# Kernel optimization log

Measured on AMD Instinct MI355X. Metric: run time of the kernel, lower is better.

## Reference

```python
import jax, jax.numpy as jnp
import numpy as np

B, N, D, H, FF, K, L = 8, 4096, 128, 8, 512, 16, 2
DH = D // H
EPS = 1e-5


def setup_inputs() -> dict:
    key = jax.random.key(0)
    ks = jax.random.split(key, 32)
    s = 0.02
    inp = {
        "x": jax.random.normal(ks[0], (B, N, 8), dtype=jnp.float32),
        "xyz_w": jax.random.normal(ks[1], (D, 3), jnp.float32) * s,
        "xyz_b": jnp.zeros((D,), jnp.float32),
        "ohe_w": jax.random.normal(ks[2], (D, 5), jnp.float32) * s,
        "ohe_b": jnp.zeros((D,), jnp.float32),
        # per-layer transformer params stacked on leading L axis
        "in_proj_w": jax.random.normal(ks[3], (L, 3 * D, D), jnp.float32) * s,
        "in_proj_b": jnp.zeros((L, 3 * D), jnp.float32),
        "out_proj_w": jax.random.normal(ks[4], (L, D, D), jnp.float32) * s,
        "out_proj_b": jnp.zeros((L, D), jnp.float32),
        "ln1_w": jnp.ones((L, D), jnp.float32),
        "ln1_b": jnp.zeros((L, D), jnp.float32),
        "lin1_w": jax.random.normal(ks[5], (L, FF, D), jnp.float32) * s,
        "lin1_b": jnp.zeros((L, FF), jnp.float32),
        "lin2_w": jax.random.normal(ks[6], (L, D, FF), jnp.float32) * s,
        "lin2_b": jnp.zeros((L, D), jnp.float32),
        "ln2_w": jnp.ones((L, D), jnp.float32),
        "ln2_b": jnp.zeros((L, D), jnp.float32),
        "fc1_w": jax.random.normal(ks[7], (FF, D), jnp.float32) * s,
        "fc1_b": jnp.zeros((FF,), jnp.float32),
        "fc2_w": jax.random.normal(ks[8], (1, FF), jnp.float32) * s,
        "fc2_b": jnp.zeros((1,), jnp.float32),
    }
    return inp


def _layer_norm(x, w, b):
    m = jnp.mean(x, -1, keepdims=True)
    v = jnp.mean((x - m) ** 2, -1, keepdims=True)
    return (x - m) * jax.lax.rsqrt(v + EPS) * w + b


def _knn_attention(xyz, feat):
    # squared euclidean distances preserve top-k ordering of cdist(p=2)
    d2 = jnp.sum((xyz[:, :, None, :] - xyz[:, None, :, :]) ** 2, -1)  # [B,N,N]
    _, idx = jax.lax.top_k(-d2, K + 1)  # ascending distance
    idx = idx[..., 1:]  # drop self -> [B,N,K]
    knn = jax.vmap(lambda f, i: f[i])(feat, idx)  # [B,N,K,D]
    scale = 1.0 / np.sqrt(D)
    scores = jnp.einsum('bnd,bnkd->bnk', feat, knn) * scale
    w = jax.nn.softmax(scores, -1)
    return jnp.einsum('bnk,bnkd->bnd', w, knn)


def _mha(x, in_w, in_b, out_w, out_b):
    qkv = x @ in_w.T + in_b  # [B,N,3D]
    q, k, v = jnp.split(qkv, 3, axis=-1)
    def heads(t):
        return t.reshape(B, N, H, DH).transpose(0, 2, 1, 3)  # [B,H,N,DH]
    q, k, v = heads(q), heads(k), heads(v)
    scores = jnp.einsum('bhqd,bhkd->bhqk', q, k) / np.sqrt(DH)
    a = jax.nn.softmax(scores, -1)
    o = jnp.einsum('bhqk,bhkd->bhqd', a, v).transpose(0, 2, 1, 3).reshape(B, N, D)
    return o @ out_w.T + out_b


def reference(x, xyz_w, xyz_b, ohe_w, ohe_b, in_proj_w, in_proj_b, out_proj_w,
              out_proj_b, ln1_w, ln1_b, lin1_w, lin1_b, lin2_w, lin2_b,
              ln2_w, ln2_b, fc1_w, fc1_b, fc2_w, fc2_b):
    xyz = x[:, :, :3]
    ohe = x[:, :, 3:8]
    feat = (xyz @ xyz_w.T + xyz_b) + (ohe @ ohe_w.T + ohe_b)  # [B,N,D]
    h = _knn_attention(xyz, feat)
    # post-norm TransformerEncoder (PyTorch default, relu, no dropout at eval)
    for l in range(L):
        a = _mha(h, in_proj_w[l], in_proj_b[l], out_proj_w[l], out_proj_b[l])
        h = _layer_norm(h + a, ln1_w[l], ln1_b[l])
        f = jax.nn.relu(h @ lin1_w[l].T + lin1_b[l]) @ lin2_w[l].T + lin2_b[l]
        h = _layer_norm(h + f, ln2_w[l], ln2_b[l])
    pooled = jnp.mean(h, axis=1)  # [B,D]
    out = jax.nn.sigmoid(jax.nn.relu(pooled @ fc1_w.T + fc1_b) @ fc2_w.T + fc2_b)
    return out
```

## Files before the change

### kernel.cpp

```cpp
#include <hip/hip_runtime.h>

#define Bq 8
#define Nq 4096
#define Dq 128
#define Hq 8
#define FFq 512
#define KNNq 16
#define Lq 2
#define DHq 16
#define EPSq 1e-5f

typedef _Float16 half4 __attribute__((ext_vector_type(4)));
typedef _Float16 half2t __attribute__((ext_vector_type(2)));
typedef float v4f __attribute__((ext_vector_type(4)));

static __device__ __forceinline__ half2t pkrtz(float a, float b) {
    return __builtin_bit_cast(half2t, __builtin_amdgcn_cvt_pkrtz(a, b));
}

__global__ __launch_bounds__(256) void prep_kernel(const float* __restrict__ x,
                                                   const float* __restrict__ xyz_w,
                                                   const float* __restrict__ xyz_b,
                                                   const float* __restrict__ ohe_w,
                                                   const float* __restrict__ ohe_b,
                                                   _Float16* __restrict__ feat16,
                                                   const float* __restrict__ ipw,
                                                   const float* __restrict__ opw,
                                                   const float* __restrict__ l1w,
                                                   const float* __restrict__ l2w,
                                                   _Float16* __restrict__ wb) {
    int bid = blockIdx.x;
    if (bid < 16384) {
        int i = bid * 256 + threadIdx.x;
        int d = i & 127;
        int t = i >> 7;
        const float* xr = x + (size_t)t * 8;
        float s = xyz_b[d] + ohe_b[d];
        s += xr[0] * xyz_w[d * 3 + 0] + xr[1] * xyz_w[d * 3 + 1] + xr[2] * xyz_w[d * 3 + 2];
        s += xr[3] * ohe_w[d * 5 + 0] + xr[4] * ohe_w[d * 5 + 1] + xr[5] * ohe_w[d * 5 + 2]
           + xr[6] * ohe_w[d * 5 + 3] + xr[7] * ohe_w[d * 5 + 4];
        feat16[i] = (_Float16)s;
    } else {
        int i = (bid - 16384) * 256 + threadIdx.x;
        float v;
        if (i < 98304) v = ipw[i];
        else if (i < 131072) v = opw[i - 98304];
        else if (i < 262144) v = l1w[i - 131072];
        else v = l2w[i - 262144];
        wb[i] = (_Float16)v;
    }
}

__global__ __launch_bounds__(512) void knn_kernel(const float* __restrict__ x, int* __restrict__ idx) {
    __shared__ __attribute__((aligned(16))) float sx[Nq];
    __shared__ __attribute__((aligned(16))) float sy[Nq];
    __shared__ __attribute__((aligned(16))) float sz[Nq];
    unsigned int (*md)[17] = (unsigned int (*)[17])sx;
    int b = blockIdx.y;
    int tid = threadIdx.x;
    for (int p = tid; p < Nq; p += 512) {
        const float* xr = x + ((size_t)b * Nq + p) * 8;
        sx[p] = xr[0]; sy[p] = xr[1]; sz[p] = xr[2];
    }
    __syncthreads();
    int qi = tid >> 3;
    int part = tid & 7;
    int n = blockIdx.x * 64 + qi;
    float qx = sx[n], qy = sy[n], qz = sz[n];
    unsigned int top[16];
#pragma unroll
    for (int i = 0; i < 16; i++) top[i] = 0xFFFFFFFFu;
    int j0 = part * 512;
    int rot = part;
    for (int bb = 0; bb < 32; bb++) {
        unsigned int c[16];
#pragma unroll
        for (int u = 0; u < 16; u++) {
            int j = j0 + ((bb * 16 + rot + u) & 511);
            float px = sx[j], py = sy[j], pz = sz[j];
            float dx = qx - px, dy = qy - py, dz = qz - pz;
            float d2 = fmaf(dx, dx, fmaf(dy, dy, dz * dz));
            c[u] = (__float_as_uint(d2) & 0xFFFFF000u) | (unsigned int)j;
        }
#pragma unroll
        for (int kk = 2; kk <= 16; kk <<= 1) {
#pragma unroll
            for (int jj = 16 >> 1; jj > 0; jj >>= 1) {
                if (jj < kk) {
#pragma unroll
                    for (int i = 0; i < 16; i++) {
                        int l = i ^ jj;
                        if (l > i) {
                            unsigned int a0 = c[i], b0 = c[l];
                            unsigned int mn = a0 < b0 ? a0 : b0;
                            unsigned int mx = a0 < b0 ? b0 : a0;
                            bool up = ((i & kk) == 0);
                            c[i] = up ? mn : mx;
                            c[l] = up ? mx : mn;
                        }
                    }
                }
            }
        }
#pragma unroll
        for (int i = 0; i < 16; i++) {
            unsigned int a0 = top[i], b0 = c[15 - i];
            top[i] = a0 < b0 ? a0 : b0;
        }
#pragma unroll
        for (int d = 8; d >= 1; d >>= 1) {
#pragma unroll
            for (int i = 0; i < 16; i++) {
                if ((i & d) == 0) {
                    int l = i | d;
                    unsigned int a0 = top[i], b0 = top[l];
                    top[i] = a0 < b0 ? a0 : b0;
                    top[l] = a0 < b0 ? b0 : a0;
                }
            }
        }
    }
    __syncthreads();
#pragma unroll
    for (int i = 0; i < 16; i++) md[tid][i] = top[i];
    md[tid][16] = 0xFFFFFFFFu;
    __syncthreads();
    if (part == 0) {
        unsigned long long pall = 0;
        int* op = idx + ((size_t)b * Nq + n) * KNNq;
        int base_row = qi * 8;
#pragma unroll
        for (int s = 0; s < KNNq + 1; s++) {
            unsigned int best = 0xFFFFFFFFu; int bp = 0;
#pragma unroll
            for (int p2 = 0; p2 < 8; p2++) {
                unsigned int ptr = (unsigned int)((pall >> (p2 * 5)) & 31u);
                unsigned int v = md[base_row + p2][ptr];
                if (v < best) { best = v; bp = p2; }
            }
            if (s > 0) op[s - 1] = (int)(best & 4095u);
            pall += (1ull << (bp * 5));
        }
    }
}

__global__ __launch_bounds__(256, 4) void knn_attn_kernel(const _Float16* __restrict__ feat16,
                                                          const int* __restrict__ idx,
                                                          _Float16* __restrict__ h16) {
    int wave = threadIdx.x >> 6;
    int lane = threadIdx.x & 63;
    int token = blockIdx.x * 4 + wave;
    int b = token >> 12;
    half2t fh = ((const half2t*)(feat16 + (size_t)token * Dq))[lane];
    float2 f = make_float2((float)fh[0], (float)fh[1]);
    const int* ip = idx + (size_t)token * KNNq;
    int jj[KNNq];
#pragma unroll
    for (int k = 0; k < KNNq; k++) jj[k] = ip[k];
    float2 g[KNNq];
#pragma unroll
    for (int k = 0; k < KNNq; k++) {
        half2t gh = ((const half2t*)(feat16 + (((size_t)b << 12) + jj[k]) * Dq))[lane];
        g[k] = make_float2((float)gh[0], (float)gh[1]);
    }
    float sc[KNNq];
#pragma unroll
    for (int k = 0; k < KNNq; k++) {
        float p = f.x * g[k].x + f.y * g[k].y;
#pragma unroll
        for (int m = 1; m < 64; m <<= 1) p += __shfl_xor(p, m);
        sc[k] = p * 0.088388347648318447f;
    }
    float mx = sc[0];
#pragma unroll
    for (int k = 1; k < KNNq; k++) mx = fmaxf(mx, sc[k]);
    float sum = 0.f;
#pragma unroll
    for (int k = 0; k < KNNq; k++) { sc[k] = __expf(sc[k] - mx); sum += sc[k]; }
    float inv = 1.f / sum;
    float o0 = 0.f, o1 = 0.f;
#pragma unroll
    for (int k = 0; k < KNNq; k++) { o0 += sc[k] * g[k].x; o1 += sc[k] * g[k].y; }
    ((half2t*)(h16 + (size_t)token * Dq))[lane] = pkrtz(o0 * inv, o1 * inv);
}

template <int MODE>
__global__ __launch_bounds__(256) void hgemm_kernel(const _Float16* __restrict__ A,
                                                    const _Float16* __restrict__ W,
                                                    const float* __restrict__ bias,
                                                    void* __restrict__ Cout,
                                                    int M, int Nc, int K) {
    int tid = threadIdx.x;
    int lane = tid & 63, w = tid >> 6;
    int l15 = lane & 15, l4 = lane >> 4;
    int m0 = blockIdx.y * 64 + w * 16;
    int n0 = blockIdx.x * 64;
    const _Float16* Ap = A + (size_t)(m0 + l15) * K + l4 * 4;
    const _Float16* Wp = W + (size_t)(n0 + l15) * K + l4 * 4;
    v4f acc[4] = {{0.f, 0.f, 0.f, 0.f}, {0.f, 0.f, 0.f, 0.f}, {0.f, 0.f, 0.f, 0.f}, {0.f, 0.f, 0.f, 0.f}};
    for (int ks = 0; ks < K; ks += 16) {
        half4 af = *(const half4*)(Ap + ks);
#pragma unroll
        for (int nt = 0; nt < 4; nt++) {
            half4 wf = *(const half4*)(Wp + (size_t)nt * 16 * K + ks);
            acc[nt] = __builtin_amdgcn_mfma_f32_16x16x16f16(wf, af, acc[nt], 0, 0, 0);
        }
    }
    int m = m0 + l15;
#pragma unroll
    for (int nt = 0; nt < 4; nt++) {
        int nb = n0 + nt * 16 + l4 * 4;
        float4 bv = *(const float4*)(bias + nb);
        float v0 = acc[nt][0] + bv.x, v1 = acc[nt][1] + bv.y;
        float v2 = acc[nt][2] + bv.z, v3 = acc[nt][3] + bv.w;
        int n_base = n0 + nt * 16;
        int sel = n_base >> 7;
        if (MODE == 2 && sel == 0) {
            v0 *= 0.36067376f; v1 *= 0.36067376f; v2 *= 0.36067376f; v3 *= 0.36067376f;
        }
        half2t lo = pkrtz(v0, v1);
        half2t hi = pkrtz(v2, v3);
        half4 hv; hv[0] = lo[0]; hv[1] = lo[1]; hv[2] = hi[0]; hv[3] = hi[1];
        if (sel < 2) {
            int hh = (n_base >> 4) & 7;
            size_t base = (size_t)sel * (64ull * Nq * 16)
                        + ((size_t)((m >> 12) * 8 + hh)) * (Nq * 16)
                        + (size_t)(m & 4095) * 16 + l4 * 4;
            *(half4*)((_Float16*)Cout + base) = hv;
        } else {
            int hh = (n_base >> 4) & 7;
            size_t vb = 2ull * 64 * Nq * 16
                      + ((size_t)((m >> 12) * 8 + hh)) * (16 * Nq)
                      + (size_t)(m & 4095);
            _Float16* vp = (_Float16*)Cout + vb + (size_t)(l4 * 4) * Nq;
            vp[0 * Nq] = hv[0]; vp[1 * Nq] = hv[1]; vp[2 * Nq] = hv[2]; vp[3 * Nq] = hv[3];
        }
    }
}

__global__ __launch_bounds__(256) void flash12_kernel(const _Float16* __restrict__ pk,
                                                      _Float16* __restrict__ out16) {
    __shared__ _Float16 Ks[2][64 * 20];
    __shared__ _Float16 Vs[2][16 * 66];
    int tid = threadIdx.x;
    int lane = tid & 63, w = tid >> 6;
    int bh = blockIdx.y;
    const _Float16* Qb = pk + (size_t)bh * (Nq * 16);
    const _Float16* Kb = pk + (size_t)(64 + bh) * (Nq * 16);
    const _Float16* Vt = pk + 2ull * 64 * Nq * 16 + (size_t)bh * (16 * Nq);
    int q0 = blockIdx.x * 128 + w * 32;
    int l15 = lane & 15, l4 = lane >> 4;

    half4 qfA = *(const half4*)(Qb + (size_t)(q0 + l15) * 16 + l4 * 4);
    half4 qfB = *(const half4*)(Qb + (size_t)(q0 + 16 + l15) * 16 + l4 * 4);

    int sr = tid >> 2, sc = tid & 3;
    int vd = tid >> 4, vj = (tid & 15) * 4;
    const _Float16* Kg = Kb + (size_t)sr * 16 + sc * 4;
    const _Float16* Vg = Vt + (size_t)vd * Nq + vj;

    *(half4*)(Ks[0] + sr * 20 + sc * 4) = *(const half4*)(Kg);
    *(half4*)(Vs[0] + vd * 66 + vj) = *(const half4*)(Vg);
    __syncthreads();

    v4f oA = {0.f, 0.f, 0.f, 0.f}, oB = {0.f, 0.f, 0.f, 0.f};
    v4f lacA = {0.f, 0.f, 0.f, 0.f}, lacB = {0.f, 0.f, 0.f, 0.f};
    half4 ones;
    ones[0] = ones[1] = ones[2] = ones[3] = (_Float16)1.0f;

    for (int kt = 0; kt < Nq / 64; kt++) {
        int cur = kt & 1, nxt = cur ^ 1;
        if (kt < Nq / 64 - 1) {
            *(half4*)(Ks[nxt] + sr * 20 + sc * 4) = *(const half4*)(Kg + (size_t)(kt + 1) * 64 * 16);
            *(half4*)(Vs[nxt] + vd * 66 + vj) = *(const half4*)(Vg + (kt + 1) * 64);
        }
        half4 kf[4];
#pragma unroll
        for (int g = 0; g < 4; g++)
            kf[g] = *(const half4*)(Ks[cur] + (g * 16 + l15) * 20 + l4 * 4);
        v4f SA[4], SB[4];
#pragma unroll
        for (int g = 0; g < 4; g++) {
            SA[g] = __builtin_amdgcn_mfma_f32_16x16x16f16(kf[g], qfA, (v4f){0.f, 0.f, 0.f, 0.f}, 0, 0, 0);
            SB[g] = __builtin_amdgcn_mfma_f32_16x16x16f16(kf[g], qfB, (v4f){0.f, 0.f, 0.f, 0.f}, 0, 0, 0);
        }
        half4 PA[4], PB[4];
#pragma unroll
        for (int g = 0; g < 4; g++) {
            float a0 = __builtin_amdgcn_exp2f(SA[g][0]);
            float a1 = __builtin_amdgcn_exp2f(SA[g][1]);
            float a2 = __builtin_amdgcn_exp2f(SA[g][2]);
            float a3 = __builtin_amdgcn_exp2f(SA[g][3]);
            half2t alo = pkrtz(a0, a1);
            half2t ahi = pkrtz(a2, a3);
            PA[g][0] = alo[0]; PA[g][1] = alo[1]; PA[g][2] = ahi[0]; PA[g][3] = ahi[1];
            float b0 = __builtin_amdgcn_exp2f(SB[g][0]);
            float b1 = __builtin_amdgcn_exp2f(SB[g][1]);
            float b2 = __builtin_amdgcn_exp2f(SB[g][2]);
            float b3 = __builtin_amdgcn_exp2f(SB[g][3]);
            half2t blo = pkrtz(b0, b1);
            half2t bhi = pkrtz(b2, b3);
            PB[g][0] = blo[0]; PB[g][1] = blo[1]; PB[g][2] = bhi[0]; PB[g][3] = bhi[1];
        }
#pragma unroll
        for (int g = 0; g < 4; g++) {
            half4 vf = *(const half4*)(Vs[cur] + l15 * 66 + g * 16 + l4 * 4);
            lacA = __builtin_amdgcn_mfma_f32_16x16x16f16(ones, PA[g], lacA, 0, 0, 0);
            oA = __builtin_amdgcn_mfma_f32_16x16x16f16(vf, PA[g], oA, 0, 0, 0);
            lacB = __builtin_amdgcn_mfma_f32_16x16x16f16(ones, PB[g], lacB, 0, 0, 0);
            oB = __builtin_amdgcn_mfma_f32_16x16x16f16(vf, PB[g], oB, 0, 0, 0);
        }
        __syncthreads();
    }
    int b = bh >> 3, hh = bh & 7;
    {
        float inv = 1.f / lacA[0];
        int row = q0 + l15;
        half2t lo = pkrtz(oA[0] * inv, oA[1] * inv);
        half2t hi = pkrtz(oA[2] * inv, oA[3] * inv);
        half4 hv; hv[0] = lo[0]; hv[1] = lo[1]; hv[2] = hi[0]; hv[3] = hi[1];
        *(half4*)(out16 + ((size_t)(b * Nq + row)) * Dq + hh * 16 + l4 * 4) = hv;
    }
    {
        float inv = 1.f / lacB[0];
        int row = q0 + 16 + l15;
        half2t lo = pkrtz(oB[0] * inv, oB[1] * inv);
        half2t hi = pkrtz(oB[2] * inv, oB[3] * inv);
        half4 hv; hv[0] = lo[0]; hv[1] = lo[1]; hv[2] = hi[0]; hv[3] = hi[1];
        *(half4*)(out16 + ((size_t)(b * Nq + row)) * Dq + hh * 16 + l4 * 4) = hv;
    }
}

template <int LAST>
__global__ __launch_bounds__(256) void oln_ffn_kernel(const _Float16* __restrict__ A,
                                                      const _Float16* __restrict__ Wo,
                                                      const float* __restrict__ bo,
                                                      const float* __restrict__ ln1w,
                                                      const float* __restrict__ ln1b,
                                                      const _Float16* __restrict__ W1,
                                                      const float* __restrict__ b1,
                                                      const _Float16* __restrict__ W2,
                                                      const float* __restrict__ b2,
                                                      const float* __restrict__ ln2w,
                                                      const float* __restrict__ ln2b,
                                                      _Float16* __restrict__ h16,
                                                      float* __restrict__ part) {
    int tid = threadIdx.x;
    int lane = tid & 63, w = tid >> 6;
    int l15 = lane & 15, l4 = lane >> 4;
    int m0 = blockIdx.x * 64 + w * 16;
    int m = m0 + l15;

    const _Float16* Ap = A + (size_t)m * 128 + l4 * 4;
    const _Float16* Wp = Wo + (size_t)l15 * 128 + l4 * 4;
    v4f acc[8] = {};
    for (int ks = 0; ks < 128; ks += 16) {
        half4 af = *(const half4*)(Ap + ks);
#pragma unroll
        for (int nt = 0; nt < 8; nt++) {
            half4 wf = *(const half4*)(Wp + (size_t)nt * 16 * 128 + ks);
            acc[nt] = __builtin_amdgcn_mfma_f32_16x16x16f16(wf, af, acc[nt], 0, 0, 0);
        }
    }
    float x[8][4];
    float psum = 0.f;
#pragma unroll
    for (int nt = 0; nt < 8; nt++) {
        int nb = nt * 16 + l4 * 4;
        float4 bv = *(const float4*)(bo + nb);
        half4 rv = *(const half4*)(h16 + (size_t)m * Dq + nb);
        x[nt][0] = acc[nt][0] + bv.x + (float)rv[0];
        x[nt][1] = acc[nt][1] + bv.y + (float)rv[1];
        x[nt][2] = acc[nt][2] + bv.z + (float)rv[2];
        x[nt][3] = acc[nt][3] + bv.w + (float)rv[3];
        psum += (x[nt][0] + x[nt][1]) + (x[nt][2] + x[nt][3]);
    }
    psum += __shfl_xor(psum, 16);
    psum += __shfl_xor(psum, 32);
    float mean = psum * (1.f / 128.f);
    float vsum = 0.f;
#pragma unroll
    for (int nt = 0; nt < 8; nt++)
#pragma unroll
        for (int r = 0; r < 4; r++) {
            x[nt][r] -= mean;
            vsum += x[nt][r] * x[nt][r];
        }
    vsum += __shfl_xor(vsum, 16);
    vsum += __shfl_xor(vsum, 32);
    float inv1 = rsqrtf(vsum * (1.f / 128.f) + EPSq);
    half4 afr[8];
#pragma unroll
    for (int nt = 0; nt < 8; nt++) {
        int nb = nt * 16 + l4 * 4;
        float4 wv = *(const float4*)(ln1w + nb);
        float4 bb = *(const float4*)(ln1b + nb);
        float y0 = x[nt][0] * inv1 * wv.x + bb.x;
        float y1 = x[nt][1] * inv1 * wv.y + bb.y;
        float y2 = x[nt][2] * inv1 * wv.z + bb.z;
        float y3 = x[nt][3] * inv1 * wv.w + bb.w;
        half2t lo = pkrtz(y0, y1);
        half2t hi = pkrtz(y2, y3);
        afr[nt][0] = lo[0]; afr[nt][1] = lo[1]; afr[nt][2] = hi[0]; afr[nt][3] = hi[1];
    }

    half4 mid[32];
#pragma unroll
    for (int c = 0; c < 8; c++) {
        v4f accm[4] = {};
#pragma unroll
        for (int t = 0; t < 8; t++) {
#pragma unroll
            for (int nt = 0; nt < 4; nt++) {
                half4 wf = *(const half4*)(W1 + (size_t)(c * 64 + nt * 16 + l15) * 128 + t * 16 + l4 * 4);
                accm[nt] = __builtin_amdgcn_mfma_f32_16x16x16f16(wf, afr[t], accm[nt], 0, 0, 0);
            }
        }
#pragma unroll
        for (int nt = 0; nt < 4; nt++) {
            float4 bv = *(const float4*)(b1 + c * 64 + nt * 16 + l4 * 4);
            float v0 = fmaxf(accm[nt][0] + bv.x, 0.f);
            float v1 = fmaxf(accm[nt][1] + bv.y, 0.f);
            float v2 = fmaxf(accm[nt][2] + bv.z, 0.f);
            float v3 = fmaxf(accm[nt][3] + bv.w, 0.f);
            half2t lo = pkrtz(v0, v1), hi = pkrtz(v2, v3);
            half4 hv; hv[0] = lo[0]; hv[1] = lo[1]; hv[2] = hi[0]; hv[3] = hi[1];
            mid[c * 4 + nt] = hv;
        }
    }
    v4f acc8[8] = {};
#pragma unroll 4
    for (int t = 0; t < 32; t++) {
#pragma unroll
        for (int nt = 0; nt < 8; nt++) {
            half4 wf = *(const half4*)(W2 + (size_t)(nt * 16 + l15) * 512 + t * 16 + l4 * 4);
            acc8[nt] = __builtin_amdgcn_mfma_f32_16x16x16f16(wf, mid[t], acc8[nt], 0, 0, 0);
        }
    }
    float x2[8][4];
    float psum2 = 0.f;
#pragma unroll
    for (int nt = 0; nt < 8; nt++) {
        int nb = nt * 16 + l4 * 4;
        float4 bv = *(const float4*)(b2 + nb);
        x2[nt][0] = acc8[nt][0] + bv.x + (float)afr[nt][0];
        x2[nt][1] = acc8[nt][1] + bv.y + (float)afr[nt][1];
        x2[nt][2] = acc8[nt][2] + bv.z + (float)afr[nt][2];
        x2[nt][3] = acc8[nt][3] + bv.w + (float)afr[nt][3];
        psum2 += (x2[nt][0] + x2[nt][1]) + (x2[nt][2] + x2[nt][3]);
    }
    psum2 += __shfl_xor(psum2, 16);
    psum2 += __shfl_xor(psum2, 32);
    float mean2 = psum2 * (1.f / 128.f);
    float vsum2 = 0.f;
#pragma unroll
    for (int nt = 0; nt < 8; nt++)
#pragma unroll
        for (int r = 0; r < 4; r++) {
            x2[nt][r] -= mean2;
            vsum2 += x2[nt][r] * x2[nt][r];
        }
    vsum2 += __shfl_xor(vsum2, 16);
    vsum2 += __shfl_xor(vsum2, 32);
    float inv2 = rsqrtf(vsum2 * (1.f / 128.f) + EPSq);
#pragma unroll
    for (int nt = 0; nt < 8; nt++) {
        int nb = nt * 16 + l4 * 4;
        float4 wv = *(const float4*)(ln2w + nb);
        float4 bb = *(const float4*)(ln2b + nb);
        x2[nt][0] = x2[nt][0] * inv2 * wv.x + bb.x;
        x2[nt][1] = x2[nt][1] * inv2 * wv.y + bb.y;
        x2[nt][2] = x2[nt][2] * inv2 * wv.z + bb.z;
        x2[nt][3] = x2[nt][3] * inv2 * wv.w + bb.w;
        if (!LAST) {
            half2t lo = pkrtz(x2[nt][0], x2[nt][1]);
            half2t hi = pkrtz(x2[nt][2], x2[nt][3]);
            half4 hv2; hv2[0] = lo[0]; hv2[1] = lo[1]; hv2[2] = hi[0]; hv2[3] = hi[1];
            *(half4*)(h16 + (size_t)m * Dq + nb) = hv2;
        }
    }
    if (LAST) {
#pragma unroll
        for (int nt = 0; nt < 8; nt++)
#pragma unroll
            for (int r = 0; r < 4; r++) {
                float v = x2[nt][r];
                v += __shfl_xor(v, 1);
                v += __shfl_xor(v, 2);
                v += __shfl_xor(v, 4);
                v += __shfl_xor(v, 8);
                x2[nt][r] = v;
            }
        if (l15 == 0) {
            float* pp = part + ((size_t)blockIdx.x * 4 + w) * Dq;
#pragma unroll
            for (int nt = 0; nt < 8; nt++)
#pragma unroll
                for (int r = 0; r < 4; r++)
                    pp[nt * 16 + l4 * 4 + r] = x2[nt][r];
        }
    }
}

__global__ __launch_bounds__(512) void head_kernel(const float* __restrict__ part,
                                                   const float* __restrict__ fc1_w, const float* __restrict__ fc1_b,
                                                   const float* __restrict__ fc2_w, const float* __restrict__ fc2_b,
                                                   float* __restrict__ out) {
    __shared__ float psh[Dq];
    __shared__ float red[512];
    int b = blockIdx.x, f = threadIdx.x;
    if (f < Dq) {
        float s = 0.f;
        for (int c = 0; c < 256; c++) s += part[((size_t)b * 256 + c) * Dq + f];
        psh[f] = s * (1.f / 4096.f);
    }
    __syncthreads();
    const float* wr = fc1_w + (size_t)f * Dq;
    float s = fc1_b[f];
    for (int d = 0; d < Dq; d++) s += psh[d] * wr[d];
    red[f] = fmaxf(s, 0.f) * fc2_w[f];
    __syncthreads();
    for (int st = 256; st > 0; st >>= 1) {
        if (f < st) red[f] += red[f + st];
        __syncthreads();
    }
    if (f == 0) out[b] = 1.f / (1.f + __expf(-(red[0] + fc2_b[0])));
}

extern "C" void kernel_launch(void* const* d_in, const int* in_sizes, int n_in,
                              void* d_out, int out_size, void* d_ws, size_t ws_size,
                              hipStream_t stream) {
    const float* x        = (const float*)d_in[0];
    const float* xyz_w    = (const float*)d_in[1];
    const float* xyz_b    = (const float*)d_in[2];
    const float* ohe_w    = (const float*)d_in[3];
    const float* ohe_b    = (const float*)d_in[4];
    const float* in_proj_w  = (const float*)d_in[5];
    const float* in_proj_b  = (const float*)d_in[6];
    const float* out_proj_w = (const float*)d_in[7];
    const float* out_proj_b = (const float*)d_in[8];
    const float* ln1_w    = (const float*)d_in[9];
    const float* ln1_b    = (const float*)d_in[10];
    const float* lin1_w   = (const float*)d_in[11];
    const float* lin1_b   = (const float*)d_in[12];
    const float* lin2_w   = (const float*)d_in[13];
    const float* lin2_b   = (const float*)d_in[14];
    const float* ln2_w    = (const float*)d_in[15];
    const float* ln2_b    = (const float*)d_in[16];
    const float* fc1_w    = (const float*)d_in[17];
    const float* fc1_b    = (const float*)d_in[18];
    const float* fc2_w    = (const float*)d_in[19];
    const float* fc2_b    = (const float*)d_in[20];
    float* outp = (float*)d_out;

    char* ws = (char*)d_ws;
    size_t off = 0;
    auto alloc = [&](size_t bytes) { void* p = ws + off; off += (bytes + 255) & ~255ULL; return p; };
    _Float16*  feat16 = (_Float16*)alloc((size_t)Bq * Nq * Dq * 2);
    _Float16*  h16    = (_Float16*)alloc((size_t)Bq * Nq * Dq * 2);
    _Float16*  abuf16 = (_Float16*)alloc((size_t)Bq * Nq * Dq * 2);
    _Float16*  pkb    = (_Float16*)alloc(3ull * 64 * Nq * 16 * 2);
    _Float16*  wb     = (_Float16*)alloc(393216ull * 2);
    int*       idx    = (int*)alloc((size_t)Bq * Nq * KNNq * 4);
    float*     part   = (float*)alloc(2048ull * Dq * 4);
    if (off > ws_size) return;

    const _Float16* wip16 = wb;
    const _Float16* wop16 = wb + 98304;
    const _Float16* wl116 = wb + 131072;
    const _Float16* wl216 = wb + 262144;

    int M = Bq * Nq;

    prep_kernel<<<16384 + 1536, 256, 0, stream>>>(x, xyz_w, xyz_b, ohe_w, ohe_b, feat16,
                                                  in_proj_w, out_proj_w, lin1_w, lin2_w, wb);
    knn_kernel<<<dim3(Nq / 64, Bq), 512, 0, stream>>>(x, idx);
    knn_attn_kernel<<<M / 4, 256, 0, stream>>>(feat16, idx, h16);

    for (int l = 0; l < Lq; l++) {
        hgemm_kernel<2><<<dim3(384 / 64, M / 64), 256, 0, stream>>>(
            h16, wip16 + (size_t)l * 384 * 128, in_proj_b + l * 384, pkb, M, 384, 128);
        flash12_kernel<<<dim3(Nq / 128, Bq * Hq), 256, 0, stream>>>(pkb, abuf16);
        if (l == 0) {
            oln_ffn_kernel<0><<<M / 64, 256, 0, stream>>>(
                abuf16, wop16, out_proj_b,
                ln1_w, ln1_b,
                wl116, lin1_b, wl216, lin2_b,
                ln2_w, ln2_b, h16, part);
        } else {
            oln_ffn_kernel<1><<<M / 64, 256, 0, stream>>>(
                abuf16, wop16 + (size_t)l * 128 * 128, out_proj_b + l * 128,
                ln1_w + l * 128, ln1_b + l * 128,
                wl116 + (size_t)l * 512 * 128, lin1_b + l * 512,
                wl216 + (size_t)l * 128 * 512, lin2_b + l * 128,
                ln2_w + l * 128, ln2_b + l * 128, h16, part);
        }
    }

    head_kernel<<<Bq, 512, 0, stream>>>(part, fc1_w, fc1_b, fc2_w, fc2_b, outp);
}
```

Before: 1.010 ms.

## Give each wave private K/V LDS buffers and drop block barriers in flash attention

The flash attention kernel now gives each of the four waves its own double-buffered K/V tiles in shared memory. Each wave stages the full 64-key tile itself, so the per-tile __syncthreads block barrier goes away. The main loop is unrolled by two with explicit stage/compute macros that alternate the two buffers. The cost is four times the global/L2 loads and four times the LDS footprint per block. Correctness now depends on LDS ordering within a wavefront, since there is no explicit barrier.

```diff
diff --git a/kernel.cpp b/kernel.cpp
--- a/kernel.cpp
+++ b/kernel.cpp
@@ -238,10 +238,10 @@
     }
 }
 
-__global__ __launch_bounds__(256) void flash12_kernel(const _Float16* __restrict__ pk,
+__global__ __launch_bounds__(256) void flash17_kernel(const _Float16* __restrict__ pk,
                                                       _Float16* __restrict__ out16) {
-    __shared__ _Float16 Ks[2][64 * 20];
-    __shared__ _Float16 Vs[2][16 * 66];
+    __shared__ _Float16 KsAll[4][2][64 * 20];
+    __shared__ _Float16 VsAll[4][2][16 * 66];
     int tid = threadIdx.x;
     int lane = tid & 63, w = tid >> 6;
     int bh = blockIdx.y;
@@ -254,64 +254,92 @@
     half4 qfA = *(const half4*)(Qb + (size_t)(q0 + l15) * 16 + l4 * 4);
     half4 qfB = *(const half4*)(Qb + (size_t)(q0 + 16 + l15) * 16 + l4 * 4);
 
-    int sr = tid >> 2, sc = tid & 3;
-    int vd = tid >> 4, vj = (tid & 15) * 4;
-    const _Float16* Kg = Kb + (size_t)sr * 16 + sc * 4;
-    const _Float16* Vg = Vt + (size_t)vd * Nq + vj;
-
-    *(half4*)(Ks[0] + sr * 20 + sc * 4) = *(const half4*)(Kg);
-    *(half4*)(Vs[0] + vd * 66 + vj) = *(const half4*)(Vg);
-    __syncthreads();
+    const _Float16* KgRow = Kb + (size_t)lane * 16;
+    int vdr = lane >> 3, vseg = lane & 7;
+    const _Float16* VgRow0 = Vt + (size_t)vdr * Nq + vseg * 8;
+    const _Float16* VgRow1 = Vt + (size_t)(vdr + 8) * Nq + vseg * 8;
+
+    _Float16 (*Ks)[64 * 20] = KsAll[w];
+    _Float16 (*Vs)[16 * 66] = VsAll[w];
+
+#define FLASH_STAGE(buf, tile) {                                              \
+        const _Float16* kg = KgRow + (size_t)(tile) * (64 * 16);              \
+        half4 ka = *(const half4*)(kg + 0);                                   \
+        half4 kb2 = *(const half4*)(kg + 4);                                  \
+        half4 kc = *(const half4*)(kg + 8);                                   \
+        half4 kd4 = *(const half4*)(kg + 12);                                 \
+        const _Float16* vg0 = VgRow0 + (tile) * 64;                           \
+        const _Float16* vg1 = VgRow1 + (tile) * 64;                           \
+        half4 va = *(const half4*)(vg0 + 0);                                  \
+        half4 vb2 = *(const half4*)(vg0 + 4);                                 \
+        half4 vc = *(const half4*)(vg1 + 0);                                  \
+        half4 vd4 = *(const half4*)(vg1 + 4);                                 \
+        _Float16* kw = Ks[buf] + lane * 20;                                   \
+        *(half4*)(kw + 0) = ka;  *(half4*)(kw + 4) = kb2;                     \
+        *(half4*)(kw + 8) = kc;  *(half4*)(kw + 12) = kd4;                    \
+        _Float16* vw0 = Vs[buf] + vdr * 66 + vseg * 8;                        \
+        *(half4*)(vw0 + 0) = va; *(half4*)(vw0 + 4) = vb2;                    \
+        _Float16* vw1 = Vs[buf] + (vdr + 8) * 66 + vseg * 8;                  \
+        *(half4*)(vw1 + 0) = vc; *(half4*)(vw1 + 4) = vd4;                    \
+    }
+
+#define FLASH_COMPUTE(buf) {                                                                              \
+        const _Float16* Kc = Ks[buf];                                                                     \
+        const _Float16* Vc = Vs[buf];                                                                     \
+        half4 kf[4];                                                                                      \
+        _Pragma("unroll")                                                                                 \
+        for (int g = 0; g < 4; g++)                                                                       \
+            kf[g] = *(const half4*)(Kc + (g * 16 + l15) * 20 + l4 * 4);                                   \
+        v4f SA[4], SB[4];                                                                                 \
+        _Pragma("unroll")                                                                                 \
+        for (int g = 0; g < 4; g++) {                                                                     \
+            SA[g] = __builtin_amdgcn_mfma_f32_16x16x16f16(kf[g], qfA, (v4f){0.f, 0.f, 0.f, 0.f}, 0, 0, 0);\
+            SB[g] = __builtin_amdgcn_mfma_f32_16x16x16f16(kf[g], qfB, (v4f){0.f, 0.f, 0.f, 0.f}, 0, 0, 0);\
+        }                                                                                                 \
+        half4 PA[4], PB[4];                                                                               \
+        _Pragma("unroll")                                                                                 \
+        for (int g = 0; g < 4; g++) {                                                                     \
+            float a0 = __builtin_amdgcn_exp2f(SA[g][0]);                                                  \
+            float a1 = __builtin_amdgcn_exp2f(SA[g][1]);                                                  \
+            float a2 = __builtin_amdgcn_exp2f(SA[g][2]);                                                  \
+            float a3 = __builtin_amdgcn_exp2f(SA[g][3]);                                                  \
+            half2t alo = pkrtz(a0, a1);                                                                   \
+            half2t ahi = pkrtz(a2, a3);                                                                   \
+            PA[g][0] = alo[0]; PA[g][1] = alo[1]; PA[g][2] = ahi[0]; PA[g][3] = ahi[1];                   \
+            float b0 = __builtin_amdgcn_exp2f(SB[g][0]);                                                  \
+            float b1 = __builtin_amdgcn_exp2f(SB[g][1]);                                                  \
+            float b2 = __builtin_amdgcn_exp2f(SB[g][2]);                                                  \
+            float b3 = __builtin_amdgcn_exp2f(SB[g][3]);                                                  \
+            half2t blo = pkrtz(b0, b1);                                                                   \
+            half2t bhi = pkrtz(b2, b3);                                                                   \
+            PB[g][0] = blo[0]; PB[g][1] = blo[1]; PB[g][2] = bhi[0]; PB[g][3] = bhi[1];                   \
+        }                                                                                                 \
+        _Pragma("unroll")                                                                                 \
+        for (int g = 0; g < 4; g++) {                                                                     \
+            half4 vf = *(const half4*)(Vc + l15 * 66 + g * 16 + l4 * 4);                                  \
+            lacA = __builtin_amdgcn_mfma_f32_16x16x16f16(ones, PA[g], lacA, 0, 0, 0);                     \
+            oA = __builtin_amdgcn_mfma_f32_16x16x16f16(vf, PA[g], oA, 0, 0, 0);                           \
+            lacB = __builtin_amdgcn_mfma_f32_16x16x16f16(ones, PB[g], lacB, 0, 0, 0);                     \
+            oB = __builtin_amdgcn_mfma_f32_16x16x16f16(vf, PB[g], oB, 0, 0, 0);                           \
+        }                                                                                                 \
+    }
 
     v4f oA = {0.f, 0.f, 0.f, 0.f}, oB = {0.f, 0.f, 0.f, 0.f};
     v4f lacA = {0.f, 0.f, 0.f, 0.f}, lacB = {0.f, 0.f, 0.f, 0.f};
     half4 ones;
     ones[0] = ones[1] = ones[2] = ones[3] = (_Float16)1.0f;
 
-    for (int kt = 0; kt < Nq / 64; kt++) {
-        int cur = kt & 1, nxt = cur ^ 1;
-        if (kt < Nq / 64 - 1) {
-            *(half4*)(Ks[nxt] + sr * 20 + sc * 4) = *(const half4*)(Kg + (size_t)(kt + 1) * 64 * 16);
-            *(half4*)(Vs[nxt] + vd * 66 + vj) = *(const half4*)(Vg + (kt + 1) * 64);
-        }
-        half4 kf[4];
-#pragma unroll
-        for (int g = 0; g < 4; g++)
-            kf[g] = *(const half4*)(Ks[cur] + (g * 16 + l15) * 20 + l4 * 4);
-        v4f SA[4], SB[4];
-#pragma unroll
-        for (int g = 0; g < 4; g++) {
-            SA[g] = __builtin_amdgcn_mfma_f32_16x16x16f16(kf[g], qfA, (v4f){0.f, 0.f, 0.f, 0.f}, 0, 0, 0);
-            SB[g] = __builtin_amdgcn_mfma_f32_16x16x16f16(kf[g], qfB, (v4f){0.f, 0.f, 0.f, 0.f}, 0, 0, 0);
-        }
-        half4 PA[4], PB[4];
-#pragma unroll
-        for (int g = 0; g < 4; g++) {
-            float a0 = __builtin_amdgcn_exp2f(SA[g][0]);
-            float a1 = __builtin_amdgcn_exp2f(SA[g][1]);
-            float a2 = __builtin_amdgcn_exp2f(SA[g][2]);
-            float a3 = __builtin_amdgcn_exp2f(SA[g][3]);
-            half2t alo = pkrtz(a0, a1);
-            half2t ahi = pkrtz(a2, a3);
-            PA[g][0] = alo[0]; PA[g][1] = alo[1]; PA[g][2] = ahi[0]; PA[g][3] = ahi[1];
-            float b0 = __builtin_amdgcn_exp2f(SB[g][0]);
-            float b1 = __builtin_amdgcn_exp2f(SB[g][1]);
-            float b2 = __builtin_amdgcn_exp2f(SB[g][2]);
-            float b3 = __builtin_amdgcn_exp2f(SB[g][3]);
-            half2t blo = pkrtz(b0, b1);
-            half2t bhi = pkrtz(b2, b3);
-            PB[g][0] = blo[0]; PB[g][1] = blo[1]; PB[g][2] = bhi[0]; PB[g][3] = bhi[1];
-        }
-#pragma unroll
-        for (int g = 0; g < 4; g++) {
-            half4 vf = *(const half4*)(Vs[cur] + l15 * 66 + g * 16 + l4 * 4);
-            lacA = __builtin_amdgcn_mfma_f32_16x16x16f16(ones, PA[g], lacA, 0, 0, 0);
-            oA = __builtin_amdgcn_mfma_f32_16x16x16f16(vf, PA[g], oA, 0, 0, 0);
-            lacB = __builtin_amdgcn_mfma_f32_16x16x16f16(ones, PB[g], lacB, 0, 0, 0);
-            oB = __builtin_amdgcn_mfma_f32_16x16x16f16(vf, PB[g], oB, 0, 0, 0);
-        }
-        __syncthreads();
-    }
+    FLASH_STAGE(0, 0);
+    const int NT = Nq / 64;
+    for (int kt = 0; kt < NT; kt += 2) {
+        FLASH_STAGE(1, kt + 1);
+        FLASH_COMPUTE(0);
+        if (kt + 2 < NT) FLASH_STAGE(0, kt + 2);
+        FLASH_COMPUTE(1);
+    }
+#undef FLASH_STAGE
+#undef FLASH_COMPUTE
+
     int b = bh >> 3, hh = bh & 7;
     {
         float inv = 1.f / lacA[0];
@@ -580,7 +608,7 @@
     for (int l = 0; l < Lq; l++) {
         hgemm_kernel<2><<<dim3(384 / 64, M / 64), 256, 0, stream>>>(
             h16, wip16 + (size_t)l * 384 * 128, in_proj_b + l * 384, pkb, M, 384, 128);
-        flash12_kernel<<<dim3(Nq / 128, Bq * Hq), 256, 0, stream>>>(pkb, abuf16);
+        flash17_kernel<<<dim3(Nq / 128, Bq * Hq), 256, 0, stream>>>(pkb, abuf16);
         if (l == 0) {
             oln_ffn_kernel<0><<<M / 64, 256, 0, stream>>>(
                 abuf16, wop16, out_proj_b,
```

Result: slower. 1.625 ms (+60.9%).
